# Performance work log

Measured on AMD Instinct MI355X. Metric: run time of the kernel, lower is better.

## Reference

```python
import jax, jax.numpy as jnp
import numpy as np
from jax import lax

B, L, D_MODEL = 2, 1024, 1024
EXPAND, D_STATE, D_CONV = 2, 16, 4
D_INNER = EXPAND * D_MODEL
DT_RANK = D_MODEL // 16  # ceil(1024/16) = 64
D_FF = 4 * D_MODEL


def setup_inputs() -> dict:
    key = jax.random.key(0)
    ks = jax.random.split(key, 20)
    s = lambda *sh: 1.0 / np.sqrt(sh[-1])
    inp = {
        "x": jax.random.normal(ks[0], (B, L, D_MODEL), jnp.float32),
        "ln1_w": jnp.ones((D_MODEL,), jnp.float32),
        "ln1_b": jnp.zeros((D_MODEL,), jnp.float32),
        "W_in": jax.random.normal(ks[1], (2 * D_INNER, D_MODEL), jnp.float32) * s(D_MODEL),
        "conv_w": jax.random.normal(ks[2], (D_INNER, D_CONV), jnp.float32) * s(D_CONV),
        "conv_b": jnp.zeros((D_INNER,), jnp.float32),
        "W_xproj": jax.random.normal(ks[3], (DT_RANK + 2 * D_STATE, D_INNER), jnp.float32) * s(D_INNER),
        "W_dt": jax.random.normal(ks[4], (D_INNER, DT_RANK), jnp.float32) * s(DT_RANK),
        "b_dt": jax.random.uniform(ks[5], (D_INNER,), jnp.float32, -4.0, -2.0),  # dt bias ~ small softplus
        "A_log": jnp.log(jnp.broadcast_to(jnp.arange(1, D_STATE + 1, dtype=jnp.float32), (D_INNER, D_STATE))),
        "D": jnp.ones((D_INNER,), jnp.float32),
        "W_out": jax.random.normal(ks[6], (D_MODEL, D_INNER), jnp.float32) * s(D_INNER),
        "ln2_w": jnp.ones((D_MODEL,), jnp.float32),
        "ln2_b": jnp.zeros((D_MODEL,), jnp.float32),
        "W1": jax.random.normal(ks[7], (D_FF, D_MODEL), jnp.float32) * s(D_MODEL),
        "b1": jnp.zeros((D_FF,), jnp.float32),
        "W2": jax.random.normal(ks[8], (D_MODEL, D_FF), jnp.float32) * s(D_FF),
        "b2": jnp.zeros((D_MODEL,), jnp.float32),
    }
    return inp


def _layernorm(x, w, b, eps=1e-5):
    mu = jnp.mean(x, axis=-1, keepdims=True)
    var = jnp.var(x, axis=-1, keepdims=True)
    return (x - mu) * lax.rsqrt(var + eps) * w + b


def _mamba(h, W_in, conv_w, conv_b, W_xproj, W_dt, b_dt, A_log, D, W_out):
    # in_proj -> [B, L, 2*d_inner]
    xz = jnp.einsum("bld,ed->ble", h, W_in)
    u, z = xz[..., :D_INNER], xz[..., D_INNER:]
    # causal depthwise conv over time
    uc = jnp.transpose(u, (0, 2, 1))  # [B, d_inner, L]
    uc = lax.conv_general_dilated(
        uc, conv_w[:, None, :], window_strides=(1,), padding=[(D_CONV - 1, 0)],
        dimension_numbers=("NCH", "OIH", "NCH"), feature_group_count=D_INNER)
    uc = jax.nn.silu(uc + conv_b[None, :, None])
    u = jnp.transpose(uc, (0, 2, 1))  # [B, L, d_inner]
    # input-dependent dt, B, C
    x_db = jnp.einsum("bld,ed->ble", u, W_xproj)
    dt = jax.nn.softplus(jnp.einsum("blr,dr->bld", x_db[..., :DT_RANK], W_dt) + b_dt)
    Bm = x_db[..., DT_RANK:DT_RANK + D_STATE]  # [B, L, d_state]
    Cm = x_db[..., DT_RANK + D_STATE:]         # [B, L, d_state]
    A = -jnp.exp(A_log)                        # [d_inner, d_state]

    def step(hst, t):
        dt_t, B_t, C_t, u_t = t  # [B,d_inner], [B,ds], [B,ds], [B,d_inner]
        dA = jnp.exp(dt_t[:, :, None] * A)                       # [B,d_inner,d_state]
        hst = dA * hst + dt_t[:, :, None] * B_t[:, None, :] * u_t[:, :, None]
        y_t = jnp.einsum("bds,bs->bd", hst, C_t)
        return hst, y_t

    h0 = jnp.zeros((u.shape[0], D_INNER, D_STATE), u.dtype)
    xs = (jnp.swapaxes(dt, 0, 1), jnp.swapaxes(Bm, 0, 1), jnp.swapaxes(Cm, 0, 1), jnp.swapaxes(u, 0, 1))
    _, ys = lax.scan(step, h0, xs)
    y = jnp.swapaxes(ys, 0, 1) + u * D  # skip term D*u
    y = y * jax.nn.silu(z)
    return jnp.einsum("ble,de->bld", y, W_out)


def reference(x, ln1_w, ln1_b, W_in, conv_w, conv_b, W_xproj, W_dt, b_dt, A_log, D,
              W_out, ln2_w, ln2_b, W1, b1, W2, b2):
    x = x + _mamba(_layernorm(x, ln1_w, ln1_b), W_in, conv_w, conv_b, W_xproj, W_dt, b_dt, A_log, D, W_out)
    h = _layernorm(x, ln2_w, ln2_b)
    ffn = jnp.einsum("blf,df->bld", jax.nn.relu(jnp.einsum("bld,fd->blf", h, W1) + b1), W2) + b2
    return x + ffn
```

## Files before the change

kernel.cpp:

```cpp
#include <hip/hip_runtime.h>

typedef unsigned short u16;
typedef unsigned int   u32;
typedef short   bf16x8 __attribute__((ext_vector_type(8)));
typedef float   f32x4  __attribute__((ext_vector_type(4)));
typedef u16     u16x4  __attribute__((ext_vector_type(4)));

__device__ __forceinline__ u16 f2b(float f) {
    u32 u = __builtin_bit_cast(u32, f);
    u32 r = u + 0x7FFFu + ((u >> 16) & 1u);
    return (u16)(r >> 16);
}
__device__ __forceinline__ float b2f(u16 h) {
    u32 u = ((u32)h) << 16;
    return __builtin_bit_cast(float, u);
}
__device__ __forceinline__ u16x4 f4_to_b4(float4 v) {
    u16x4 o; o.x = f2b(v.x); o.y = f2b(v.y); o.z = f2b(v.z); o.w = f2b(v.w);
    return o;
}

__device__ __forceinline__ float fexp2(float x) {
    float r;
    asm("v_exp_f32 %0, %1" : "=v"(r) : "v"(x));
    return r;
}
__device__ __forceinline__ float flog2(float x) {
    float r;
    asm("v_log_f32 %0, %1" : "=v"(r) : "v"(x));
    return r;
}

template <int CTRL>
__device__ __forceinline__ float dpp_add(float p) {
    int pi = __builtin_bit_cast(int, p);
    int q  = __builtin_amdgcn_update_dpp(pi, pi, CTRL, 0xF, 0xF, false);
    return p + __builtin_bit_cast(float, q);
}
#define DPP_XOR1 0xB1
#define DPP_XOR2 0x4E
#define DPP_HMIR 0x141
#define DPP_MIR  0x140

#define MROWS   2048
#define NSEG    16
#define SEGT    64
#define L2E     1.44269504088896340736f
#define LN2     0.69314718055994530942f

#define GLDS(g, l) __builtin_amdgcn_global_load_lds(                      \
    (const __attribute__((address_space(1))) void*)(g),                   \
    (__attribute__((address_space(3))) void*)(l), 16, 0, 0)

__global__ __launch_bounds__(256) void cvt_all(const float* __restrict__ W_in,
                                               const float* __restrict__ W_out,
                                               const float* __restrict__ W1,
                                               const float* __restrict__ W2,
                                               const float* __restrict__ W_dt,
                                               u16* __restrict__ Winb,
                                               u16* __restrict__ Woutb,
                                               u16* __restrict__ W1b,
                                               u16* __restrict__ W2b,
                                               u16* __restrict__ Wdtb) {
    const int i = blockIdx.x * 256 + threadIdx.x;
    const float* src; u16* dst; int off;
    if (i < 1048576)      { src = W_in;  dst = Winb;  off = i; }
    else if (i < 1572864) { src = W_out; dst = Woutb; off = i - 1048576; }
    else if (i < 2621440) { src = W1;    dst = W1b;   off = i - 1572864; }
    else if (i < 3670016) { src = W2;    dst = W2b;   off = i - 2621440; }
    else                  { src = W_dt;  dst = Wdtb;  off = i - 3670016; }
    float4 v = ((const float4*)src)[off];
    ((u16x4*)dst)[off] = f4_to_b4(v);
}

__global__ __launch_bounds__(256) void pad_xproj_kernel(const float* __restrict__ in,
                                                        u16* __restrict__ out) {
    int i = blockIdx.x * 256 + threadIdx.x;
    int r = i >> 9, c4 = i & 511;
    float4 v = make_float4(0.f, 0.f, 0.f, 0.f);
    if (r < 96) v = ((const float4*)(in + (size_t)r * 2048))[c4];
    ((u16x4*)(out + (size_t)r * 2048))[c4] = f4_to_b4(v);
}

__global__ __launch_bounds__(256) void ln_kernel(const float* __restrict__ x,
                                                 const float* __restrict__ w,
                                                 const float* __restrict__ b,
                                                 u16* __restrict__ out) {
    const int row = blockIdx.x;
    const int tid = threadIdx.x;
    const float4 v = ((const float4*)(x + (size_t)row * 1024))[tid];
    float s = v.x + v.y + v.z + v.w;
    float q = v.x * v.x + v.y * v.y + v.z * v.z + v.w * v.w;
#pragma unroll
    for (int off = 1; off < 64; off <<= 1) {
        s += __shfl_xor(s, off, 64);
        q += __shfl_xor(q, off, 64);
    }
    __shared__ float ss[4], qq[4];
    const int wave = tid >> 6;
    if ((tid & 63) == 0) { ss[wave] = s; qq[wave] = q; }
    __syncthreads();
    s = ss[0] + ss[1] + ss[2] + ss[3];
    q = qq[0] + qq[1] + qq[2] + qq[3];
    const float mean = s * (1.f / 1024.f);
    const float var  = q * (1.f / 1024.f) - mean * mean;
    const float rstd = rsqrtf(var + 1e-5f);
    const float4 wv = ((const float4*)w)[tid];
    const float4 bv = ((const float4*)b)[tid];
    float4 o;
    o.x = (v.x - mean) * rstd * wv.x + bv.x;
    o.y = (v.y - mean) * rstd * wv.y + bv.y;
    o.z = (v.z - mean) * rstd * wv.z + bv.z;
    o.w = (v.w - mean) * rstd * wv.w + bv.w;
    ((u16x4*)(out + (size_t)row * 1024))[tid] = f4_to_b4(o);
}

__global__ __launch_bounds__(256) void conv_kernel(const u16* __restrict__ xzu,
                                                   const float* __restrict__ cw,
                                                   const float* __restrict__ cb,
                                                   u16* __restrict__ utl) {
    const int idx = blockIdx.x * 256 + threadIdx.x;
    const int row = idx >> 9;
    const int d4  = idx & 511;
    const int d   = d4 * 4;
    const int bb  = row >> 10;
    const int t   = row & 1023;
    float w0[4], w1[4], w2[4], w3[4];
    *(float4*)w0 = ((const float4*)cw)[d + 0];
    *(float4*)w1 = ((const float4*)cw)[d + 1];
    *(float4*)w2 = ((const float4*)cw)[d + 2];
    *(float4*)w3 = ((const float4*)cw)[d + 3];
    float4 a = ((const float4*)cb)[d4];
#pragma unroll
    for (int j = 0; j < 4; ++j) {
        const int tt = t - 3 + j;
        if (tt >= 0) {
            const u16x4 uv = *(const u16x4*)(xzu + ((size_t)(bb * 1024 + tt)) * 2048 + d);
            a.x += b2f(uv.x) * w0[j];
            a.y += b2f(uv.y) * w1[j];
            a.z += b2f(uv.z) * w2[j];
            a.w += b2f(uv.w) * w3[j];
        }
    }
    float4 o;
    o.x = a.x / (1.f + __expf(-a.x));
    o.y = a.y / (1.f + __expf(-a.y));
    o.z = a.z / (1.f + __expf(-a.z));
    o.w = a.w / (1.f + __expf(-a.w));
    *(u16x4*)(utl + (((size_t)(d >> 4)) * 2048 + row) * 16 + (d & 15)) = f4_to_b4(o);
}

template <int EPI>
__global__ __launch_bounds__(512) void gemm_tb(const u16* __restrict__ A,
                                               const u16* __restrict__ Bw,
                                               void* __restrict__ Cptr,
                                               void* __restrict__ Cptr2,
                                               const float* __restrict__ bias,
                                               int M, int N, int K, int KS) {
    const int nbm = gridDim.x, nbn = gridDim.y;
    const int nwg = nbm * nbn;
    const int id  = blockIdx.x + nbm * blockIdx.y;
    const int sw  = (nwg >= 8) ? ((id & 7) * (nwg >> 3) + (id >> 3)) : id;
    const int bm  = sw % nbm, bn = sw / nbm;

    __shared__ u16 Asm[3][128 * 32];
    __shared__ u16 Bsm[3][128 * 32];
    const int tid  = threadIdx.x;
    const int kz   = blockIdx.z;
    const int lane = tid & 63;
    const int wave = tid >> 6;
    const int wm   = wave >> 1, wn = wave & 1;
    const u16* Ag = A  + (size_t)bm * 128 * K;
    const u16* Bg = Bw + (size_t)bn * 128 * K;
    const int r0 = tid >> 2;
    const int sg = (tid & 3) * 8;
    const int k0 = kz * KS;
    const int nk = KS >> 5;
    const int fr = lane & 15, fk = (lane >> 4) * 8;

#define STG(bf, kk)                                                            \
    {                                                                          \
        const int kof = k0 + (kk) * 32;                                        \
        GLDS(Ag + (size_t)r0 * K + kof + sg, &Asm[bf][tid * 8]);               \
        GLDS(Bg + (size_t)r0 * K + kof + sg, &Bsm[bf][tid * 8]);               \
    }

    f32x4 acc[2][4] = {};
    STG(0, 0); STG(1, 1);
    int buf = 0;
    for (int k = 0; k < nk; ++k) {
        if (k < nk - 1) asm volatile("s_waitcnt vmcnt(2)" ::: "memory");
        else            asm volatile("s_waitcnt vmcnt(0)" ::: "memory");
        __builtin_amdgcn_s_barrier();
        bf16x8 a[2], b[4];
#pragma unroll
        for (int m = 0; m < 2; ++m)
            a[m] = *(const bf16x8*)&Asm[buf][(wm * 32 + m * 16 + fr) * 32 + fk];
#pragma unroll
        for (int n = 0; n < 4; ++n)
            b[n] = *(const bf16x8*)&Bsm[buf][(wn * 64 + n * 16 + fr) * 32 + fk];
        if (k + 2 < nk) {
            const int slot = (buf + 2) % 3;
            STG(slot, k + 2);
        }
#pragma unroll
        for (int m = 0; m < 2; ++m)
#pragma unroll
            for (int n = 0; n < 4; ++n)
                acc[m][n] = __builtin_amdgcn_mfma_f32_16x16x32_bf16(a[m], b[n], acc[m][n], 0, 0, 0);
        buf = (buf == 2) ? 0 : buf + 1;
    }
#undef STG

    const int fq = lane >> 4;
#pragma unroll
    for (int m = 0; m < 2; ++m) {
#pragma unroll
        for (int n = 0; n < 4; ++n) {
            const int row0 = bm * 128 + wm * 32 + m * 16 + fq * 4;
            const int col  = bn * 128 + wn * 64 + n * 16 + fr;
#pragma unroll
            for (int j = 0; j < 4; ++j) {
                float v = acc[m][n][j];
                if constexpr (EPI == 3) {
                    v += bias[col];
                    ((u16*)Cptr)[(size_t)(row0 + j) * N + col] = f2b(fmaxf(v, 0.f));
                } else if constexpr (EPI == 5) {
                    if (col < 2048) {
                        ((u16*)Cptr)[(size_t)(row0 + j) * 2048 + col] = f2b(v);
                    } else {
                        const float sv = v / (1.f + __expf(-v));
                        const int zc = col - 2048;
                        ((u16*)Cptr2)[(((size_t)(zc >> 4)) * 2048 + row0 + j) * 16 + (zc & 15)]
                            = f2b(sv);
                    }
                } else {
                    ((float*)Cptr)[(size_t)kz * M * N + (size_t)(row0 + j) * N + col] = v;
                }
            }
        }
    }
}

__global__ __launch_bounds__(256) void gemm_xp(const u16* __restrict__ utl,
                                               const u16* __restrict__ Bw,
                                               float* __restrict__ part) {
    const int nwg = 16;
    const int id  = blockIdx.x;
    const int sw  = (id & 7) * (nwg >> 3) + (id >> 3);
    const int bm  = sw;
    __shared__ u16 Asm[3][128 * 32];
    __shared__ u16 Bsm[3][128 * 32];
    const int tid  = threadIdx.x;
    const int kz   = blockIdx.z;
    const int lane = tid & 63;
    const int wave = tid >> 6;
    const int wm   = wave >> 1, wn = wave & 1;
    const u16* Bg = Bw;
    const int r0 = tid >> 2;
    const int pc = tid & 3;
    const int sg = pc * 8;
    const int k0 = kz * 256;
    const int fr = lane & 15, fk = (lane >> 4) * 8;

#define STGX(bf, kk)                                                                     \
    {                                                                                    \
        const int kof = k0 + (kk) * 32;                                                  \
        const int kc  = kof >> 4;                                                        \
        GLDS(utl + ((size_t)(kc + (pc >> 1)) * 2048 + bm * 128 + r0) * 16 + (pc & 1) * 8,\
             &Asm[bf][tid * 8]);                                                         \
        GLDS(utl + ((size_t)(kc + (pc >> 1)) * 2048 + bm * 128 + r0 + 64) * 16 + (pc & 1) * 8,\
             &Asm[bf][(tid + 256) * 8]);                                                 \
        GLDS(Bg + (size_t)r0 * 2048 + kof + sg, &Bsm[bf][tid * 8]);                      \
        GLDS(Bg + (size_t)(r0 + 64) * 2048 + kof + sg, &Bsm[bf][(tid + 256) * 8]);       \
    }

    f32x4 acc[4][4] = {};
    STGX(0, 0); STGX(1, 1);
    int buf = 0;
    const int nk = 8;
    for (int k = 0; k < nk; ++k) {
        if (k < nk - 1) asm volatile("s_waitcnt vmcnt(4)" ::: "memory");
        else            asm volatile("s_waitcnt vmcnt(0)" ::: "memory");
        __builtin_amdgcn_s_barrier();
        bf16x8 a[4], b[4];
#pragma unroll
        for (int m = 0; m < 4; ++m)
            a[m] = *(const bf16x8*)&Asm[buf][(wm * 64 + m * 16 + fr) * 32 + fk];
#pragma unroll
        for (int n = 0; n < 4; ++n)
            b[n] = *(const bf16x8*)&Bsm[buf][(wn * 64 + n * 16 + fr) * 32 + fk];
        if (k + 2 < nk) {
            const int slot = (buf + 2) % 3;
            STGX(slot, k + 2);
        }
#pragma unroll
        for (int m = 0; m < 4; ++m)
#pragma unroll
            for (int n = 0; n < 4; ++n)
                acc[m][n] = __builtin_amdgcn_mfma_f32_16x16x32_bf16(a[m], b[n], acc[m][n], 0, 0, 0);
        buf = (buf == 2) ? 0 : buf + 1;
    }
#undef STGX

    const int fq = lane >> 4;
    float* Cp = part + (size_t)kz * MROWS * 128;
#pragma unroll
    for (int m = 0; m < 4; ++m) {
#pragma unroll
        for (int n = 0; n < 4; ++n) {
            const int row0 = bm * 128 + wm * 64 + m * 16 + fq * 4;
            const int col  = wn * 64 + n * 16 + fr;
#pragma unroll
            for (int j = 0; j < 4; ++j)
                Cp[(size_t)(row0 + j) * 128 + col] = acc[m][n][j];
        }
    }
}

__global__ __launch_bounds__(256) void xproj_combine(const float* __restrict__ part,
                                                     u16* __restrict__ xdbr,
                                                     float* __restrict__ bcp,
                                                     float* __restrict__ bpk) {
    int i = blockIdx.x * 256 + threadIdx.x;
    int row = i >> 5, c4 = i & 31;
    if (c4 >= 24) return;
    float4 s = make_float4(0.f, 0.f, 0.f, 0.f);
#pragma unroll
    for (int p = 0; p < 8; ++p) {
        float4 v = ((const float4*)(part + (size_t)p * MROWS * 128 + (size_t)row * 128))[c4];
        s.x += v.x; s.y += v.y; s.z += v.z; s.w += v.w;
    }
    if (c4 < 16) {
        ((u16x4*)(xdbr + (size_t)row * 64))[c4] = f4_to_b4(s);
    } else {
        const int e0 = (c4 - 16) * 4;
        float sv[4] = {s.x, s.y, s.z, s.w};
#pragma unroll
        for (int j = 0; j < 4; ++j) {
            const int e = e0 + j;
            const int st  = (e < 16) ? e : (e - 16);
            const int isc = (e < 16) ? 0 : 1;
            bcp[(size_t)(row >> 1) * 64 + st * 4 + (row & 1) * 2 + isc] = sv[j];
            if (e < 16)
                bpk[(size_t)(row >> 1) * 32 + st * 2 + (row & 1)] = sv[j];
        }
    }
}

__device__ __forceinline__ void compute_dtu_tile(const u16* __restrict__ xdbr,
                                                 const u16* __restrict__ Wdtb,
                                                 const float* __restrict__ b_dt,
                                                 const u16* __restrict__ utile,
                                                 float* __restrict__ du_s,
                                                 size_t t0, int d0, int w, int l) {
    const int fr = l & 15, fk = (l >> 4) * 8;
    const bf16x8 a0 = *(const bf16x8*)(xdbr + (t0 + w * 16 + fr) * 64 + fk);
    const bf16x8 a1 = *(const bf16x8*)(xdbr + (t0 + w * 16 + fr) * 64 + 32 + fk);
    const bf16x8 b0 = *(const bf16x8*)(Wdtb + (size_t)(d0 + fr) * 64 + fk);
    const bf16x8 b1 = *(const bf16x8*)(Wdtb + (size_t)(d0 + fr) * 64 + 32 + fk);
    const float bdt = b_dt[d0 + fr];
    f32x4 acc = {};
    acc = __builtin_amdgcn_mfma_f32_16x16x32_bf16(a0, b0, acc, 0, 0, 0);
    acc = __builtin_amdgcn_mfma_f32_16x16x32_bf16(a1, b1, acc, 0, 0, 0);
#pragma unroll
    for (int j = 0; j < 4; ++j) {
        const int row = w * 16 + (l >> 4) * 4 + j;
        float v = acc[j] + bdt;
        const float sp = flog2(1.f + fexp2(v * L2E)) * LN2;
        v = (v > 20.f) ? v : sp;
        const float uval = b2f(utile[(t0 + row) * 16 + fr]);
        float2 dv; dv.x = v; dv.y = v * uval;
        *(float2*)&du_s[(row >> 1) * 66 + fr * 4 + (row & 1) * 2] = dv;
    }
}

__device__ __forceinline__ void stage_bc(const float* __restrict__ bcp,
                                         float* __restrict__ bc_s,
                                         size_t p0, int w, int l) {
    const int pr = (w << 3) + (l >> 4);
    const int pc = (l & 15) << 2;
    GLDS(bcp + (p0 + pr) * 64 + pc,     &bc_s[(w << 9)]);
    GLDS(bcp + (p0 + pr + 4) * 64 + pc, &bc_s[(w << 9) + 256]);
}

__global__ __launch_bounds__(256) void scan_pass1(const u16* __restrict__ xdbr,
                                                  const u16* __restrict__ Wdtb,
                                                  const float* __restrict__ b_dt,
                                                  const u16* __restrict__ utl,
                                                  const float* __restrict__ bpk,
                                                  const float* __restrict__ A_log,
                                                  float* __restrict__ Qarr,
                                                  float* __restrict__ Sarr) {
    __shared__ __align__(16) float du_s[32 * 66];
    __shared__ __align__(16) float bp_s[32 * 32];

    const int tid = threadIdx.x;
    const int l   = tid & 63;
    const int w   = tid >> 6;
    const int s   = l & 15;
    const int g   = (w << 2) | (l >> 4);
    const int d0  = blockIdx.x << 4;
    const int b   = blockIdx.y;
    const int seg = blockIdx.z;
    const int d   = d0 + g;
    const size_t t0 = (size_t)b * 1024 + (size_t)seg * SEGT;
    const u16* utile = utl + (size_t)(d0 >> 4) * 2048 * 16;

    GLDS(bpk + ((t0 >> 1) + (tid >> 3)) * 32 + ((tid & 7) << 2), &bp_s[w << 8]);
    compute_dtu_tile(xdbr, Wdtb, b_dt, utile, du_s, t0, d0, w, l);

    const float As2 = -__expf(A_log[d * 16 + s]) * L2E;
    asm volatile("s_waitcnt vmcnt(0) lgkmcnt(0)" ::: "memory");
    __builtin_amdgcn_s_barrier();

    float Q = 0.f, S = 0.f;
#pragma unroll 8
    for (int t2 = 0; t2 < 32; ++t2) {
        const float4 du4 = *(const float4*)&du_s[t2 * 66 + g * 4];
        const float2 Bp  = *(const float2*)&bp_s[t2 * 32 + s * 2];
        S += du4.x;
        Q = fexp2(du4.x * As2) * Q + du4.y * Bp.x;
        S += du4.z;
        Q = fexp2(du4.z * As2) * Q + du4.w * Bp.y;
    }
    Qarr[(((size_t)seg * 2 + b) * 2048 + d) * 16 + s] = Q;
    if (s == 0) Sarr[((size_t)seg * 2 + b) * 2048 + d] = S;
}

__global__ __launch_bounds__(256) void scan_prefix(const float* __restrict__ Qarr,
                                                   const float* __restrict__ Sarr,
                                                   const float* __restrict__ A_log,
                                                   float* __restrict__ H0) {
    const int tid = threadIdx.x;
    const int d   = (blockIdx.x << 4) + (tid >> 4);
    const int s   = tid & 15;
    const int b   = blockIdx.y;
    const float As2 = -__expf(A_log[d * 16 + s]) * L2E;
    float h = 0.f;
#pragma unroll
    for (int i = 0; i < NSEG; ++i) {
        const size_t base = ((size_t)i * 2 + b) * 2048 + d;
        H0[base * 16 + s] = h;
        h = fexp2(As2 * Sarr[base]) * h + Qarr[base * 16 + s];
    }
}

__global__ __launch_bounds__(256) void scan_pass2(const u16* __restrict__ xdbr,
                                                  const u16* __restrict__ Wdtb,
                                                  const float* __restrict__ b_dt,
                                                  const u16* __restrict__ utl,
                                                  const float* __restrict__ bcp,
                                                  const u16* __restrict__ zst,
                                                  const float* __restrict__ A_log,
                                                  const float* __restrict__ Dp,
                                                  const float* __restrict__ H0,
                                                  u16* __restrict__ ymul) {
    __shared__ __align__(16) float du_s[32 * 66];
    __shared__ __align__(16) float bc_s[32 * 64];

    const int tid = threadIdx.x;
    const int l   = tid & 63;
    const int w   = tid >> 6;
    const int s   = l & 15;
    const int g   = (w << 2) | (l >> 4);
    const int d0  = blockIdx.x << 4;
    const int b   = blockIdx.y;
    const int seg = blockIdx.z;
    const int d   = d0 + g;
    const size_t t0 = (size_t)b * 1024 + (size_t)seg * SEGT;
    const u16* utile = utl + (size_t)(d0 >> 4) * 2048 * 16;
    const u16* ztile = zst + (size_t)(d0 >> 4) * 2048 * 16;

    stage_bc(bcp, bc_s, t0 >> 1, w, l);
    compute_dtu_tile(xdbr, Wdtb, b_dt, utile, du_s, t0, d0, w, l);

    const float As2 = -__expf(A_log[d * 16 + s]) * L2E;
    float h = H0[(((size_t)seg * 2 + b) * 2048 + d) * 16 + s];

    asm volatile("s_waitcnt vmcnt(0) lgkmcnt(0)" ::: "memory");
    __builtin_amdgcn_s_barrier();

    float pk[4];
#pragma unroll
    for (int c = 0; c < 4; ++c) {
        pk[c] = 0.f;
#pragma unroll
        for (int q = 0; q < 8; ++q) {
            const int t2 = c * 8 + q;
            const float4 du4 = *(const float4*)&du_s[t2 * 66 + g * 4];
            const float4 BC2 = *(const float4*)&bc_s[t2 * 64 + s * 4];
            h = fexp2(du4.x * As2) * h + du4.y * BC2.x;
            float p = h * BC2.y;
            p = dpp_add<DPP_XOR1>(p);
            p = dpp_add<DPP_XOR2>(p);
            p = dpp_add<DPP_HMIR>(p);
            p = dpp_add<DPP_MIR>(p);
            {
                const unsigned long long km = 0x0001000100010001ULL << (2 * q);
                asm("v_cndmask_b32 %0, %0, %1, %2" : "+v"(pk[c]) : "v"(p), "s"(km));
            }
            h = fexp2(du4.z * As2) * h + du4.w * BC2.z;
            p = h * BC2.w;
            p = dpp_add<DPP_XOR1>(p);
            p = dpp_add<DPP_XOR2>(p);
            p = dpp_add<DPP_HMIR>(p);
            p = dpp_add<DPP_MIR>(p);
            {
                const unsigned long long km = 0x0001000100010001ULL << (2 * q + 1);
                asm("v_cndmask_b32 %0, %0, %1, %2" : "+v"(pk[c]) : "v"(p), "s"(km));
            }
        }
    }

    __builtin_amdgcn_s_barrier();
    float* p_s = du_s;
#pragma unroll
    for (int c = 0; c < 4; ++c) {
        const int row = c * 16 + s;
        p_s[row * 16 + (g ^ (row & 12))] = pk[c];
    }

    asm volatile("s_waitcnt lgkmcnt(0)" ::: "memory");
    __builtin_amdgcn_s_barrier();

    {
        const int tt = tid >> 2, cc = (tid & 3) << 2;
        const float4 pv = *(const float4*)&p_s[tt * 16 + (cc ^ (tt & 12))];
        const u16x4  uv = *(const u16x4*)(utile + (t0 + tt) * 16 + cc);
        const u16x4  zs = *(const u16x4*)(ztile + (t0 + tt) * 16 + cc);
        const float4 Dv = *(const float4*)(Dp + d0 + cc);
        float4 o;
        o.x = (pv.x + b2f(uv.x) * Dv.x) * b2f(zs.x);
        o.y = (pv.y + b2f(uv.y) * Dv.y) * b2f(zs.y);
        o.z = (pv.z + b2f(uv.z) * Dv.z) * b2f(zs.z);
        o.w = (pv.w + b2f(uv.w) * Dv.w) * b2f(zs.w);
        *(u16x4*)(ymul + (t0 + tt) * 2048 + d0 + cc) = f4_to_b4(o);
    }
}

__global__ __launch_bounds__(256) void ffn2_combine(const float* __restrict__ part,
                                                    const float* __restrict__ x2,
                                                    const float* __restrict__ b2,
                                                    float* __restrict__ out) {
    int i = blockIdx.x * 256 + threadIdx.x;
    float4 s = ((const float4*)x2)[i];
    float4 bv = ((const float4*)b2)[i & 255];
    s.x += bv.x; s.y += bv.y; s.z += bv.z; s.w += bv.w;
#pragma unroll
    for (int p = 0; p < 4; ++p) {
        float4 v = ((const float4*)(part + (size_t)p * MROWS * 1024))[i];
        s.x += v.x; s.y += v.y; s.z += v.z; s.w += v.w;
    }
    ((float4*)out)[i] = s;
}

__global__ __launch_bounds__(256) void outproj_combine_ln2(const float* __restrict__ x,
                                                           const float* __restrict__ part,
                                                           const float* __restrict__ w,
                                                           const float* __restrict__ b,
                                                           float* __restrict__ x2,
                                                           u16* __restrict__ h2) {
    const int row = blockIdx.x;
    const int tid = threadIdx.x;
    float4 v = ((const float4*)(x + (size_t)row * 1024))[tid];
    float4 p0 = ((const float4*)(part + (size_t)row * 1024))[tid];
    float4 p1 = ((const float4*)(part + (size_t)MROWS * 1024 + (size_t)row * 1024))[tid];
    v.x += p0.x + p1.x; v.y += p0.y + p1.y; v.z += p0.z + p1.z; v.w += p0.w + p1.w;
    ((float4*)(x2 + (size_t)row * 1024))[tid] = v;
    float s = v.x + v.y + v.z + v.w;
    float q = v.x * v.x + v.y * v.y + v.z * v.z + v.w * v.w;
#pragma unroll
    for (int off = 1; off < 64; off <<= 1) {
        s += __shfl_xor(s, off, 64);
        q += __shfl_xor(q, off, 64);
    }
    __shared__ float ss[4], qq[4];
    const int wave = tid >> 6;
    if ((tid & 63) == 0) { ss[wave] = s; qq[wave] = q; }
    __syncthreads();
    s = ss[0] + ss[1] + ss[2] + ss[3];
    q = qq[0] + qq[1] + qq[2] + qq[3];
    const float mean = s * (1.f / 1024.f);
    const float var  = q * (1.f / 1024.f) - mean * mean;
    const float rstd = rsqrtf(var + 1e-5f);
    const float4 wv = ((const float4*)w)[tid];
    const float4 bv = ((const float4*)b)[tid];
    float4 o;
    o.x = (v.x - mean) * rstd * wv.x + bv.x;
    o.y = (v.y - mean) * rstd * wv.y + bv.y;
    o.z = (v.z - mean) * rstd * wv.z + bv.z;
    o.w = (v.w - mean) * rstd * wv.w + bv.w;
    ((u16x4*)(h2 + (size_t)row * 1024))[tid] = f4_to_b4(o);
}

extern "C" void kernel_launch(void* const* d_in, const int* in_sizes, int n_in,
                              void* d_out, int out_size, void* d_ws, size_t ws_size,
                              hipStream_t stream) {
    const float* x      = (const float*)d_in[0];
    const float* ln1_w  = (const float*)d_in[1];
    const float* ln1_b  = (const float*)d_in[2];
    const float* W_in   = (const float*)d_in[3];
    const float* conv_w = (const float*)d_in[4];
    const float* conv_b = (const float*)d_in[5];
    const float* W_xproj= (const float*)d_in[6];
    const float* W_dt   = (const float*)d_in[7];
    const float* b_dt   = (const float*)d_in[8];
    const float* A_log  = (const float*)d_in[9];
    const float* Dvec   = (const float*)d_in[10];
    const float* W_out  = (const float*)d_in[11];
    const float* ln2_w  = (const float*)d_in[12];
    const float* ln2_b  = (const float*)d_in[13];
    const float* W1     = (const float*)d_in[14];
    const float* b1     = (const float*)d_in[15];
    const float* W2     = (const float*)d_in[16];
    const float* b2     = (const float*)d_in[17];
    float* out = (float*)d_out;
    char*  ws  = (char*)d_ws;
    const size_t MB = 1024ull * 1024ull;

    u16*   h1b   = (u16*)(ws + 0);
    u16*   xzu   = (u16*)(ws + 4 * MB);
    u16*   zst   = (u16*)(ws + 12 * MB);
    u16*   utl   = (u16*)(ws + 20 * MB);
    float* parts = (float*)(ws + 28 * MB);
    float* bcp   = (float*)(ws + 36 * MB);
    u16*   xdbr  = (u16*)(ws + 36 * MB + 256 * 1024);
    u16*   Wdtb  = (u16*)(ws + 36 * MB + 512 * 1024);
    float* bpk   = (float*)(ws + 36 * MB + 768 * 1024);
    u16*   ymul  = (u16*)(ws + 37 * MB);
    float* Qarr  = (float*)(ws + 45 * MB);
    float* Sarr  = (float*)(ws + 49 * MB);
    float* H0    = (float*)(ws + 50 * MB);
    float* x2    = (float*)(ws + 54 * MB);
    u16*   Winb  = (u16*)(ws + 62 * MB);
    u16*   Woutb = (u16*)(ws + 70 * MB);
    u16*   W1b   = (u16*)(ws + 74 * MB);
    u16*   W2b   = (u16*)(ws + 82 * MB);
    u16*   Wxpb  = (u16*)(ws + 90 * MB);
    u16*   h2b   = h1b;
    float* opart = (float*)(ws + 4 * MB);
    u16*   f1    = (u16*)(ws + 4 * MB);
    float* fpart = (float*)(ws + 20 * MB);

    cvt_all<<<14464, 256, 0, stream>>>(W_in, W_out, W1, W2, W_dt,
                                       Winb, Woutb, W1b, W2b, Wdtb);
    pad_xproj_kernel<<<256, 256, 0, stream>>>(W_xproj, Wxpb);

    ln_kernel<<<2048, 256, 0, stream>>>(x, ln1_w, ln1_b, h1b);
    gemm_tb<5><<<dim3(16, 32, 1), 512, 0, stream>>>(h1b, Winb, xzu, zst, nullptr,
                                                    MROWS, 4096, 1024, 1024);
    conv_kernel<<<4096, 256, 0, stream>>>(xzu, conv_w, conv_b, utl);
    gemm_xp<<<dim3(16, 1, 8), 256, 0, stream>>>(utl, Wxpb, parts);
    xproj_combine<<<256, 256, 0, stream>>>(parts, xdbr, bcp, bpk);
    scan_pass1<<<dim3(128, 2, NSEG), 256, 0, stream>>>(xdbr, Wdtb, b_dt, utl, bpk, A_log,
                                                       Qarr, Sarr);
    scan_prefix<<<dim3(128, 2), 256, 0, stream>>>(Qarr, Sarr, A_log, H0);
    scan_pass2<<<dim3(128, 2, NSEG), 256, 0, stream>>>(xdbr, Wdtb, b_dt, utl, bcp, zst,
                                                       A_log, Dvec, H0, ymul);
    gemm_tb<10><<<dim3(16, 8, 2), 512, 0, stream>>>(ymul, Woutb, opart, nullptr, nullptr,
                                                    MROWS, 1024, 2048, 1024);
    outproj_combine_ln2<<<2048, 256, 0, stream>>>(x, opart, ln2_w, ln2_b, x2, h2b);
    gemm_tb<3><<<dim3(16, 32, 1), 512, 0, stream>>>(h2b, W1b, f1, nullptr, b1,
                                                    MROWS, 4096, 1024, 1024);
    gemm_tb<10><<<dim3(16, 8, 4), 512, 0, stream>>>(f1, W2b, fpart, nullptr, nullptr,
                                                    MROWS, 1024, 4096, 1024);
    ffn2_combine<<<2048, 256, 0, stream>>>(fpart, x2, b2, out);
}
```

Baseline: 216.2 us.

## Fuse prep kernels, stage GEMM epilogue through LDS, split out_proj K four ways

Merges the weight conversion, xproj padding and first layernorm into a single launch to cut launch overhead. The bf16 GEMM epilogues now write each wave's tile into LDS and then issue 16-byte row-contiguous global stores instead of scattered 2-byte stores. The out_proj GEMM uses split-K of 4 instead of 2 for more workgroups, with the combine kernel summing four partials. This adds extra partial-sum traffic and an LDS round trip plus a barrier in the epilogue.

```diff
diff --git a/kernel.cpp b/kernel.cpp
--- a/kernel.cpp
+++ b/kernel.cpp
@@ -5,6 +5,7 @@
 typedef short   bf16x8 __attribute__((ext_vector_type(8)));
 typedef float   f32x4  __attribute__((ext_vector_type(4)));
 typedef u16     u16x4  __attribute__((ext_vector_type(4)));
+typedef u16     u16x8  __attribute__((ext_vector_type(8)));
 
 __device__ __forceinline__ u16 f2b(float f) {
     u32 u = __builtin_bit_cast(u32, f);
@@ -52,34 +53,68 @@
     (const __attribute__((address_space(1))) void*)(g),                   \
     (__attribute__((address_space(3))) void*)(l), 16, 0, 0)
 
-__global__ __launch_bounds__(256) void cvt_all(const float* __restrict__ W_in,
-                                               const float* __restrict__ W_out,
-                                               const float* __restrict__ W1,
-                                               const float* __restrict__ W2,
-                                               const float* __restrict__ W_dt,
-                                               u16* __restrict__ Winb,
-                                               u16* __restrict__ Woutb,
-                                               u16* __restrict__ W1b,
-                                               u16* __restrict__ W2b,
-                                               u16* __restrict__ Wdtb) {
-    const int i = blockIdx.x * 256 + threadIdx.x;
-    const float* src; u16* dst; int off;
-    if (i < 1048576)      { src = W_in;  dst = Winb;  off = i; }
-    else if (i < 1572864) { src = W_out; dst = Woutb; off = i - 1048576; }
-    else if (i < 2621440) { src = W1;    dst = W1b;   off = i - 1572864; }
-    else if (i < 3670016) { src = W2;    dst = W2b;   off = i - 2621440; }
-    else                  { src = W_dt;  dst = Wdtb;  off = i - 3670016; }
-    float4 v = ((const float4*)src)[off];
-    ((u16x4*)dst)[off] = f4_to_b4(v);
-}
-
-__global__ __launch_bounds__(256) void pad_xproj_kernel(const float* __restrict__ in,
-                                                        u16* __restrict__ out) {
-    int i = blockIdx.x * 256 + threadIdx.x;
-    int r = i >> 9, c4 = i & 511;
-    float4 v = make_float4(0.f, 0.f, 0.f, 0.f);
-    if (r < 96) v = ((const float4*)(in + (size_t)r * 2048))[c4];
-    ((u16x4*)(out + (size_t)r * 2048))[c4] = f4_to_b4(v);
+__global__ __launch_bounds__(256) void prep_kernel(const float* __restrict__ W_in,
+                                                   const float* __restrict__ W_out,
+                                                   const float* __restrict__ W1,
+                                                   const float* __restrict__ W2,
+                                                   const float* __restrict__ W_dt,
+                                                   const float* __restrict__ W_xproj,
+                                                   const float* __restrict__ x,
+                                                   const float* __restrict__ ln1_w,
+                                                   const float* __restrict__ ln1_b,
+                                                   u16* __restrict__ Winb,
+                                                   u16* __restrict__ Woutb,
+                                                   u16* __restrict__ W1b,
+                                                   u16* __restrict__ W2b,
+                                                   u16* __restrict__ Wdtb,
+                                                   u16* __restrict__ Wxpb,
+                                                   u16* __restrict__ h1b) {
+    const int blk = blockIdx.x;
+    const int tid = threadIdx.x;
+    if (blk < 14464) {
+        const int i = blk * 256 + tid;
+        const float* src; u16* dst; int off;
+        if (i < 1048576)      { src = W_in;  dst = Winb;  off = i; }
+        else if (i < 1572864) { src = W_out; dst = Woutb; off = i - 1048576; }
+        else if (i < 2621440) { src = W1;    dst = W1b;   off = i - 1572864; }
+        else if (i < 3670016) { src = W2;    dst = W2b;   off = i - 2621440; }
+        else                  { src = W_dt;  dst = Wdtb;  off = i - 3670016; }
+        float4 v = ((const float4*)src)[off];
+        ((u16x4*)dst)[off] = f4_to_b4(v);
+    } else if (blk < 14464 + 256) {
+        const int i = (blk - 14464) * 256 + tid;
+        const int r = i >> 9, c4 = i & 511;
+        float4 v = make_float4(0.f, 0.f, 0.f, 0.f);
+        if (r < 96) v = ((const float4*)(W_xproj + (size_t)r * 2048))[c4];
+        ((u16x4*)(Wxpb + (size_t)r * 2048))[c4] = f4_to_b4(v);
+    } else {
+        const int row = blk - 14720;
+        const float4 v = ((const float4*)(x + (size_t)row * 1024))[tid];
+        float s = v.x + v.y + v.z + v.w;
+        float q = v.x * v.x + v.y * v.y + v.z * v.z + v.w * v.w;
+#pragma unroll
+        for (int off = 1; off < 64; off <<= 1) {
+            s += __shfl_xor(s, off, 64);
+            q += __shfl_xor(q, off, 64);
+        }
+        __shared__ float ss[4], qq[4];
+        const int wave = tid >> 6;
+        if ((tid & 63) == 0) { ss[wave] = s; qq[wave] = q; }
+        __syncthreads();
+        s = ss[0] + ss[1] + ss[2] + ss[3];
+        q = qq[0] + qq[1] + qq[2] + qq[3];
+        const float mean = s * (1.f / 1024.f);
+        const float var  = q * (1.f / 1024.f) - mean * mean;
+        const float rstd = rsqrtf(var + 1e-5f);
+        const float4 wv = ((const float4*)ln1_w)[tid];
+        const float4 bv = ((const float4*)ln1_b)[tid];
+        float4 o;
+        o.x = (v.x - mean) * rstd * wv.x + bv.x;
+        o.y = (v.y - mean) * rstd * wv.y + bv.y;
+        o.z = (v.z - mean) * rstd * wv.z + bv.z;
+        o.w = (v.w - mean) * rstd * wv.w + bv.w;
+        ((u16x4*)(h1b + (size_t)row * 1024))[tid] = f4_to_b4(o);
+    }
 }
 
 __global__ __launch_bounds__(256) void ln_kernel(const float* __restrict__ x,
@@ -163,8 +198,9 @@
     const int sw  = (nwg >= 8) ? ((id & 7) * (nwg >> 3) + (id >> 3)) : id;
     const int bm  = sw % nbm, bn = sw / nbm;
 
-    __shared__ u16 Asm[3][128 * 32];
-    __shared__ u16 Bsm[3][128 * 32];
+    __shared__ u16 SMEM[3 * 2 * 128 * 32];
+    u16* Asm = SMEM;
+    u16* Bsm = SMEM + 3 * 128 * 32;
     const int tid  = threadIdx.x;
     const int kz   = blockIdx.z;
     const int lane = tid & 63;
@@ -181,8 +217,8 @@
 #define STG(bf, kk)                                                            \
     {                                                                          \
         const int kof = k0 + (kk) * 32;                                        \
-        GLDS(Ag + (size_t)r0 * K + kof + sg, &Asm[bf][tid * 8]);               \
-        GLDS(Bg + (size_t)r0 * K + kof + sg, &Bsm[bf][tid * 8]);               \
+        GLDS(Ag + (size_t)r0 * K + kof + sg, Asm + (bf) * 4096 + tid * 8);     \
+        GLDS(Bg + (size_t)r0 * K + kof + sg, Bsm + (bf) * 4096 + tid * 8);     \
     }
 
     f32x4 acc[2][4] = {};
@@ -195,10 +231,10 @@
         bf16x8 a[2], b[4];
 #pragma unroll
         for (int m = 0; m < 2; ++m)
-            a[m] = *(const bf16x8*)&Asm[buf][(wm * 32 + m * 16 + fr) * 32 + fk];
+            a[m] = *(const bf16x8*)&Asm[buf * 4096 + (wm * 32 + m * 16 + fr) * 32 + fk];
 #pragma unroll
         for (int n = 0; n < 4; ++n)
-            b[n] = *(const bf16x8*)&Bsm[buf][(wn * 64 + n * 16 + fr) * 32 + fk];
+            b[n] = *(const bf16x8*)&Bsm[buf * 4096 + (wn * 64 + n * 16 + fr) * 32 + fk];
         if (k + 2 < nk) {
             const int slot = (buf + 2) % 3;
             STG(slot, k + 2);
@@ -213,29 +249,55 @@
 #undef STG
 
     const int fq = lane >> 4;
-#pragma unroll
-    for (int m = 0; m < 2; ++m) {
-#pragma unroll
-        for (int n = 0; n < 4; ++n) {
-            const int row0 = bm * 128 + wm * 32 + m * 16 + fq * 4;
-            const int col  = bn * 128 + wn * 64 + n * 16 + fr;
-#pragma unroll
-            for (int j = 0; j < 4; ++j) {
-                float v = acc[m][n][j];
-                if constexpr (EPI == 3) {
-                    v += bias[col];
-                    ((u16*)Cptr)[(size_t)(row0 + j) * N + col] = f2b(fmaxf(v, 0.f));
-                } else if constexpr (EPI == 5) {
-                    if (col < 2048) {
-                        ((u16*)Cptr)[(size_t)(row0 + j) * 2048 + col] = f2b(v);
+    if constexpr (EPI == 10) {
+#pragma unroll
+        for (int m = 0; m < 2; ++m)
+#pragma unroll
+            for (int n = 0; n < 4; ++n) {
+                const int row0 = bm * 128 + wm * 32 + m * 16 + fq * 4;
+                const int col  = bn * 128 + wn * 64 + n * 16 + fr;
+#pragma unroll
+                for (int j = 0; j < 4; ++j)
+                    ((float*)Cptr)[(size_t)kz * M * N + (size_t)(row0 + j) * N + col]
+                        = acc[m][n][j];
+            }
+    } else {
+        asm volatile("s_waitcnt lgkmcnt(0)" ::: "memory");
+        __builtin_amdgcn_s_barrier();
+        u16* wbuf = SMEM + wave * 2048;
+#pragma unroll
+        for (int m = 0; m < 2; ++m)
+#pragma unroll
+            for (int n = 0; n < 4; ++n)
+#pragma unroll
+                for (int j = 0; j < 4; ++j) {
+                    float v = acc[m][n][j];
+                    if constexpr (EPI == 3) {
+                        const int col = bn * 128 + wn * 64 + n * 16 + fr;
+                        v += bias[col];
+                        v = fmaxf(v, 0.f);
                     } else {
-                        const float sv = v / (1.f + __expf(-v));
-                        const int zc = col - 2048;
-                        ((u16*)Cptr2)[(((size_t)(zc >> 4)) * 2048 + row0 + j) * 16 + (zc & 15)]
-                            = f2b(sv);
+                        if (bn >= 16) v = v / (1.f + __expf(-v));
                     }
+                    wbuf[(m * 16 + fq * 4 + j) * 64 + n * 16 + fr] = f2b(v);
+                }
+        asm volatile("s_waitcnt lgkmcnt(0)" ::: "memory");
+#pragma unroll
+        for (int i = 0; i < 4; ++i) {
+            const int c   = lane + 64 * i;
+            const int row = c >> 3;
+            const int off = (c & 7) * 8;
+            const u16x8 val = *(const u16x8*)&wbuf[row * 64 + off];
+            const int row_g = bm * 128 + wm * 32 + row;
+            const int col_g = bn * 128 + wn * 64 + off;
+            if constexpr (EPI == 3) {
+                *(u16x8*)((u16*)Cptr + (size_t)row_g * N + col_g) = val;
+            } else {
+                if (bn < 16) {
+                    *(u16x8*)((u16*)Cptr + (size_t)row_g * 2048 + col_g) = val;
                 } else {
-                    ((float*)Cptr)[(size_t)kz * M * N + (size_t)(row0 + j) * N + col] = v;
+                    const int zc = col_g - 2048;
+                    *(u16x8*)((u16*)Cptr2 + ((size_t)(zc >> 4) * 2048 + row_g) * 16 + (zc & 15)) = val;
                 }
             }
         }
@@ -564,9 +626,11 @@
     const int row = blockIdx.x;
     const int tid = threadIdx.x;
     float4 v = ((const float4*)(x + (size_t)row * 1024))[tid];
-    float4 p0 = ((const float4*)(part + (size_t)row * 1024))[tid];
-    float4 p1 = ((const float4*)(part + (size_t)MROWS * 1024 + (size_t)row * 1024))[tid];
-    v.x += p0.x + p1.x; v.y += p0.y + p1.y; v.z += p0.z + p1.z; v.w += p0.w + p1.w;
+#pragma unroll
+    for (int p = 0; p < 4; ++p) {
+        float4 pv = ((const float4*)(part + (size_t)p * MROWS * 1024 + (size_t)row * 1024))[tid];
+        v.x += pv.x; v.y += pv.y; v.z += pv.z; v.w += pv.w;
+    }
     ((float4*)(x2 + (size_t)row * 1024))[tid] = v;
     float s = v.x + v.y + v.z + v.w;
     float q = v.x * v.x + v.y * v.y + v.z * v.z + v.w * v.w;
@@ -643,11 +707,10 @@
     u16*   f1    = (u16*)(ws + 4 * MB);
     float* fpart = (float*)(ws + 20 * MB);
 
-    cvt_all<<<14464, 256, 0, stream>>>(W_in, W_out, W1, W2, W_dt,
-                                       Winb, Woutb, W1b, W2b, Wdtb);
-    pad_xproj_kernel<<<256, 256, 0, stream>>>(W_xproj, Wxpb);
-
-    ln_kernel<<<2048, 256, 0, stream>>>(x, ln1_w, ln1_b, h1b);
+    prep_kernel<<<16768, 256, 0, stream>>>(W_in, W_out, W1, W2, W_dt, W_xproj,
+                                           x, ln1_w, ln1_b,
+                                           Winb, Woutb, W1b, W2b, Wdtb, Wxpb, h1b);
+
     gemm_tb<5><<<dim3(16, 32, 1), 512, 0, stream>>>(h1b, Winb, xzu, zst, nullptr,
                                                     MROWS, 4096, 1024, 1024);
     conv_kernel<<<4096, 256, 0, stream>>>(xzu, conv_w, conv_b, utl);
@@ -658,8 +721,8 @@
     scan_prefix<<<dim3(128, 2), 256, 0, stream>>>(Qarr, Sarr, A_log, H0);
     scan_pass2<<<dim3(128, 2, NSEG), 256, 0, stream>>>(xdbr, Wdtb, b_dt, utl, bcp, zst,
                                                        A_log, Dvec, H0, ymul);
-    gemm_tb<10><<<dim3(16, 8, 2), 512, 0, stream>>>(ymul, Woutb, opart, nullptr, nullptr,
-                                                    MROWS, 1024, 2048, 1024);
+    gemm_tb<10><<<dim3(16, 8, 4), 512, 0, stream>>>(ymul, Woutb, opart, nullptr, nullptr,
+                                                    MROWS, 1024, 2048, 512);
     outproj_combine_ln2<<<2048, 256, 0, stream>>>(x, opart, ln2_w, ln2_b, x2, h2b);
     gemm_tb<3><<<dim3(16, 32, 1), 512, 0, stream>>>(h2b, W1b, f1, nullptr, b1,
                                                     MROWS, 4096, 1024, 1024);
```

Result: no change. 214.8 us (median of 2 runs) (-0.6%).
